# Performance work log

Measured on AMD Instinct MI355X. Metric: run time of the kernel, lower is better.

## Reference

```python
import jax, jax.numpy as jnp
import numpy as np

D_MODEL = 1024
N_HEADS = 16
D_KEY = 64
EPS = 1e-5


def setup_inputs() -> dict:
    key = jax.random.key(0)
    ks = jax.random.split(key, 12)
    d, h, dk = D_MODEL, N_HEADS, D_KEY
    s = lambda fan_in: 1.0 / np.sqrt(fan_in)
    inp = {
        "X": jax.random.normal(ks[0], (2, 2048, d), dtype=jnp.float32),
        "Wqkv": jax.random.uniform(ks[1], (d, 3 * h * dk), jnp.float32, -s(d), s(d)),
        "bqkv": jax.random.uniform(ks[2], (3 * h * dk,), jnp.float32, -s(d), s(d)),
        "Wo": jax.random.uniform(ks[3], (h * dk, d), jnp.float32, -s(h * dk), s(h * dk)),
        "bo": jax.random.uniform(ks[4], (d,), jnp.float32, -s(h * dk), s(h * dk)),
        "W1": jax.random.uniform(ks[5], (d, 4 * d), jnp.float32, -s(d), s(d)),
        "b1": jax.random.uniform(ks[6], (4 * d,), jnp.float32, -s(d), s(d)),
        "W2": jax.random.uniform(ks[7], (4 * d, d), jnp.float32, -s(4 * d), s(4 * d)),
        "b2": jax.random.uniform(ks[8], (d,), jnp.float32, -s(4 * d), s(4 * d)),
        "ln1_g": jnp.ones((d,), jnp.float32),
        "ln1_b": jnp.zeros((d,), jnp.float32),
        "ln2_g": jnp.ones((d,), jnp.float32),
        "ln2_b": jnp.zeros((d,), jnp.float32),
    }
    return inp


def _layernorm(x, g, b):
    mu = jnp.mean(x, axis=-1, keepdims=True)
    var = jnp.var(x, axis=-1, keepdims=True)
    return (x - mu) * jax.lax.rsqrt(var + EPS) * g + b


def _block(X, Wqkv, bqkv, Wo, bo, W1, b1, W2, b2, ln1_g, ln1_b, ln2_g, ln2_b):
    B, T, _ = X.shape
    h, dk = N_HEADS, D_KEY
    # --- causal multi-head self-attention on LN(X) ---
    Xn = _layernorm(X, ln1_g, ln1_b)
    qkv = (Xn @ Wqkv + bqkv).reshape(B, T, 3, h, dk)
    q, k, v = (jnp.moveaxis(qkv, 2, 0)[i].transpose(0, 2, 1, 3) for i in range(3))  # each [B,h,T,dk]
    scores = jnp.einsum("bhqd,bhkd->bhqk", q, k) / np.sqrt(dk).astype(np.float32)
    causal = jnp.tril(jnp.ones((T, T), dtype=bool))
    scores = jnp.where(causal, scores, -jnp.inf)
    attn = jax.nn.softmax(scores, axis=-1)
    ctx = jnp.einsum("bhqk,bhkd->bhqd", attn, v)  # [B,h,T,dk]
    ctx = ctx.transpose(0, 2, 1, 3).reshape(B, T, h * dk)
    atten = ctx @ Wo + bo
    X = X + atten  # dropout is identity in eval mode
    # --- FFN on LN(X) ---
    Xn2 = _layernorm(X, ln2_g, ln2_b)
    ffn = jax.nn.relu(Xn2 @ W1 + b1) @ W2 + b2
    return X + ffn


def reference(X, Wqkv, bqkv, Wo, bo, W1, b1, W2, b2, ln1_g, ln1_b, ln2_g, ln2_b):
    return _block(X, Wqkv, bqkv, Wo, bo, W1, b1, W2, b2, ln1_g, ln1_b, ln2_g, ln2_b)
```

## Files before the change

### kernel.cpp

```cpp
#include <hip/hip_runtime.h>
#include <hip/hip_bf16.h>

typedef __hip_bfloat16 bf16;
typedef __attribute__((ext_vector_type(8))) short short8;
typedef __attribute__((ext_vector_type(4))) float f32x4;

constexpr int D     = 1024;
constexpr int T     = 2048;
constexpr int BATCH = 2;
constexpr int ROWS  = BATCH * T;
constexpr int NH    = 16;
constexpr int DKEY  = 64;
constexpr int QKVN  = 3 * D;
constexpr int FFNN  = 4 * D;

static __device__ __forceinline__ float b2f(bf16 x) { return __bfloat162float(x); }
static __device__ __forceinline__ bf16  f2b(float x) { return __float2bfloat16(x); }
static __device__ __forceinline__ float fast_exp2(float x) { return __builtin_amdgcn_exp2f(x); }
static __device__ __forceinline__ unsigned short f2bu(float x) {
    return __bfloat16_as_ushort(__float2bfloat16(x));
}
static __device__ __forceinline__ float bits2f(unsigned short u) {
    unsigned int w = (unsigned int)u << 16;
    return __builtin_bit_cast(float, w);
}

static __device__ __forceinline__ void gload_lds16(const bf16* g, unsigned short* l) {
    __builtin_amdgcn_global_load_lds(
        (const __attribute__((address_space(1))) void*)g,
        (__attribute__((address_space(3))) void*)l,
        16, 0, 0);
}

__global__ __launch_bounds__(256) void transpose_cast(const float* __restrict__ in,
                                                      bf16* __restrict__ out,
                                                      int R, int C)
{
    __shared__ float tile[32][33];
    int c0 = blockIdx.x * 32, r0 = blockIdx.y * 32;
    int tx = threadIdx.x & 31, ty = threadIdx.x >> 5;
#pragma unroll
    for (int i = 0; i < 32; i += 8)
        tile[ty + i][tx] = in[(size_t)(r0 + ty + i) * C + c0 + tx];
    __syncthreads();
#pragma unroll
    for (int i = 0; i < 32; i += 8)
        out[(size_t)(c0 + ty + i) * R + r0 + tx] = f2b(tile[tx][ty + i]);
}

template <typename TIN>
__global__ __launch_bounds__(256) void ln_kernel(const TIN* __restrict__ X,
                                                 const float* __restrict__ g,
                                                 const float* __restrict__ b,
                                                 bf16* __restrict__ out)
{
    int row = blockIdx.x;
    int tid = threadIdx.x;
    int c0  = tid * 4;
    const TIN* xr = X + (size_t)row * D;
    float v[4];
    if constexpr (__is_same(TIN, float)) {
        float4 ld = *(const float4*)(xr + c0);
        v[0] = ld.x; v[1] = ld.y; v[2] = ld.z; v[3] = ld.w;
    } else {
        uint2 raw = *(const uint2*)(xr + c0);
        v[0] = bits2f((unsigned short)(raw.x & 0xffff));
        v[1] = bits2f((unsigned short)(raw.x >> 16));
        v[2] = bits2f((unsigned short)(raw.y & 0xffff));
        v[3] = bits2f((unsigned short)(raw.y >> 16));
    }

    float s1 = v[0] + v[1] + v[2] + v[3];
    float s2 = v[0]*v[0] + v[1]*v[1] + v[2]*v[2] + v[3]*v[3];
#pragma unroll
    for (int off = 32; off; off >>= 1) {
        s1 += __shfl_xor(s1, off);
        s2 += __shfl_xor(s2, off);
    }
    __shared__ float red[8];
    int lane = tid & 63, w = tid >> 6;
    if (lane == 0) { red[w] = s1; red[4 + w] = s2; }
    __syncthreads();
    s1 = red[0] + red[1] + red[2] + red[3];
    s2 = red[4] + red[5] + red[6] + red[7];

    float mu   = s1 * (1.0f / D);
    float var  = s2 * (1.0f / D) - mu * mu;
    float rstd = rsqrtf(var + 1e-5f);

    float4 gv = *(const float4*)(g + c0);
    float4 bv = *(const float4*)(b + c0);
    ushort4 pk;
    pk.x = f2bu((v[0] - mu) * rstd * gv.x + bv.x);
    pk.y = f2bu((v[1] - mu) * rstd * gv.y + bv.y);
    pk.z = f2bu((v[2] - mu) * rstd * gv.z + bv.z);
    pk.w = f2bu((v[3] - mu) * rstd * gv.w + bv.w);
    *(ushort4*)(out + (size_t)row * D + c0) = pk;
}

template <int BM, int RELU, int RES, int OUTF32, int SPLITZ>
__global__ __launch_bounds__(256) void mfma_gemm(
    const bf16* __restrict__ A, const bf16* __restrict__ Bt,
    const float* __restrict__ bias, const void* __restrict__ resid,
    void* __restrict__ out, float* __restrict__ part,
    int M, int N, int K, int Kstride)
{
    constexpr int MT = BM / 32;
    __shared__ __align__(16) unsigned short As[2][BM * 32];
    __shared__ __align__(16) unsigned short Bs[2][128 * 32];

    int gx = gridDim.x, gy = gridDim.y;
    int lid = (blockIdx.z * gy + blockIdx.y) * gx + blockIdx.x;
    int nwg = gx * gy * gridDim.z;
    int chunk = nwg >> 3;
    int xcd = lid & 7, c = lid >> 3;
    int f;
    if ((gx & 7) == 0 && chunk % (gx * 4) == 0) {
        int band  = c / (gx * 4);
        int r     = c % (gx * 4);
        int wi    = r >> 5;
        int inner = r & 31;
        f = xcd * chunk + band * (gx * 4) + (inner >> 3) * gx + wi * 8 + (inner & 7);
    } else {
        f = xcd * chunk + c;
    }
    int bx = f % gx;
    int by = (f / gx) % gy;
    int bz = f / (gx * gy);

    int tid  = threadIdx.x;
    int m0   = by * BM, n0 = bx * 128;
    int lane = tid & 63, wave = tid >> 6;
    int wm = (wave >> 1) * (MT * 16), wn = (wave & 1) * 64;
    int c15 = lane & 15, quad = lane >> 4;

    int koff = 0;
    if constexpr (SPLITZ) koff = bz * K;

    f32x4 acc[MT][4] = {};

    int srow = lane >> 2;
    int scol = (lane & 3) * 8;
    const bf16* abase = A  + (size_t)m0 * Kstride + koff;
    const bf16* bbase = Bt + (size_t)n0 * Kstride + koff;

    auto stage = [&](int buf, int kt) {
        int ko = kt * 32;
#pragma unroll
        for (int j = 0; j < 2; ++j) {
            int r = wave * 32 + j * 16;
            gload_lds16(bbase + (size_t)(r + srow) * Kstride + ko + scol,
                        &Bs[buf][r * 32]);
        }
        if constexpr (BM == 128) {
#pragma unroll
            for (int j = 0; j < 2; ++j) {
                int r = wave * 32 + j * 16;
                gload_lds16(abase + (size_t)(r + srow) * Kstride + ko + scol,
                            &As[buf][r * 32]);
            }
        } else {
            int r = wave * 16;
            gload_lds16(abase + (size_t)(r + srow) * Kstride + ko + scol,
                        &As[buf][r * 32]);
        }
    };

    int nk = K >> 5;
    stage(0, 0);
    __syncthreads();

    for (int kt = 0; kt < nk; ++kt) {
        int buf = kt & 1;
        if (kt + 1 < nk) stage(buf ^ 1, kt + 1);

        short8 af[MT], bfr[4];
#pragma unroll
        for (int t = 0; t < MT; ++t)
            af[t]  = *(const short8*)&As[buf][(wm + t * 16 + c15) * 32 + quad * 8];
#pragma unroll
        for (int t = 0; t < 4; ++t)
            bfr[t] = *(const short8*)&Bs[buf][(wn + t * 16 + c15) * 32 + quad * 8];
#pragma unroll
        for (int mt = 0; mt < MT; ++mt)
#pragma unroll
            for (int nt = 0; nt < 4; ++nt)
                acc[mt][nt] = __builtin_amdgcn_mfma_f32_16x16x32_bf16(
                    af[mt], bfr[nt], acc[mt][nt], 0, 0, 0);

        __syncthreads();
    }

#pragma unroll
    for (int mt = 0; mt < MT; ++mt) {
#pragma unroll
        for (int nt = 0; nt < 4; ++nt) {
            f32x4 v4 = acc[mt][nt];
            int gc = n0 + wn + nt * 16 + c15;
            float bb = (!SPLITZ || bz == 0) ? bias[gc] : 0.0f;
#pragma unroll
            for (int r = 0; r < 4; ++r) {
                int gr = m0 + wm + mt * 16 + quad * 4 + r;
                float v = v4[r] + bb;
                if constexpr (RELU) v = fmaxf(v, 0.0f);
                size_t idx = (size_t)gr * N + gc;
                if constexpr (SPLITZ) {
                    if (bz == 0) {
                        v += b2f(((const bf16*)resid)[idx]);
                        ((float*)out)[idx] = v;
                    } else {
                        part[idx] = v;
                    }
                } else {
                    if constexpr (RES == 1) v += b2f(((const bf16*)resid)[idx]);
                    if constexpr (RES == 2) v += ((const float*)resid)[idx];
                    if constexpr (OUTF32) ((float*)out)[idx] = v;
                    else                  ((bf16*)out)[idx] = f2b(v);
                }
            }
        }
    }
}

__global__ __launch_bounds__(256) void add_partial(float* __restrict__ out,
                                                   const float* __restrict__ part)
{
    int i = blockIdx.x * 256 + threadIdx.x;
    f32x4 a = ((const f32x4*)out)[i];
    f32x4 p = ((const f32x4*)part)[i];
    a += p;
    ((f32x4*)out)[i] = a;
}

__global__ __launch_bounds__(256) void flash_attn(const bf16* __restrict__ qkv,
                                                  bf16* __restrict__ ctx)
{
    constexpr int KROW = 72;
    constexpr float CSC = 0.18033688011112042f;
    constexpr float MSH = 12.0f;

    __shared__ __align__(16) unsigned short Qs[64 * KROW];
    __shared__ __align__(16) unsigned short Ks[64 * KROW];
    __shared__ __align__(16) unsigned short Vt[64 * KROW];
    unsigned short* Pt = Qs;

    int bx = blockIdx.x;
    int bh = bx & 31;
    int qi = 31 - (bx >> 5);
    int h  = bh & 15, b = bh >> 4;
    int q0 = qi * 64;

    int tid = threadIdx.x, lane = tid & 63, w = tid >> 6;
    int c15 = lane & 15, quad = lane >> 4;

    const bf16* base = qkv + (size_t)b * T * QKVN;

    {
        int row = tid >> 2, qtr = tid & 3;
        const bf16* src = base + (size_t)(q0 + row) * QKVN + h * 64 + qtr * 16;
        unsigned short* dst = &Qs[row * KROW + qtr * 16];
        uint4 v0 = *(const uint4*)(src);
        uint4 v1 = *(const uint4*)(src + 8);
        *(uint4*)(dst)     = v0;
        *(uint4*)(dst + 8) = v1;
    }
    __syncthreads();

    short8 qf[2];
#pragma unroll
    for (int s = 0; s < 2; ++s)
        qf[s] = *(const short8*)&Qs[(w * 16 + c15) * KROW + s * 32 + quad * 8];

    short8 ones;
#pragma unroll
    for (int i = 0; i < 8; ++i) ones[i] = (short)0x3F80;

    f32x4 Ot[4] = {};
    f32x4 lacc  = {};

    int nkt   = q0 / 64 + 1;
    int wqmin = q0 + w * 16;

    int key = tid >> 2, seg = tid & 3;
    int keyp = (tid & 31) * 2, dk0 = (tid >> 5) * 8;

    uint4 kv0, kv1, vv0, vv1;
    {
        const bf16* ksrc = base + (size_t)key * QKVN + D + h * 64 + seg * 16;
        kv0 = *(const uint4*)ksrc;
        kv1 = *(const uint4*)(ksrc + 8);
        const bf16* vsrc = base + (size_t)keyp * QKVN + 2 * D + h * 64 + dk0;
        vv0 = *(const uint4*)vsrc;
        vv1 = *(const uint4*)(vsrc + QKVN);
    }

    for (int kt = 0; kt < nkt; ++kt) {
        int k0 = kt * 64;

        __syncthreads();
        {
            unsigned short* kd = &Ks[key * KROW + seg * 16];
            *(uint4*)kd       = kv0;
            *(uint4*)(kd + 8) = kv1;
            const unsigned short* lo = (const unsigned short*)&vv0;
            const unsigned short* hi = (const unsigned short*)&vv1;
#pragma unroll
            for (int j = 0; j < 8; ++j) {
                unsigned int pk = (unsigned int)lo[j] | ((unsigned int)hi[j] << 16);
                *(unsigned int*)&Vt[(dk0 + j) * KROW + keyp] = pk;
            }
        }
        __syncthreads();

        if (kt + 1 < nkt) {
            int k1 = k0 + 64;
            const bf16* ksrc = base + (size_t)(k1 + key) * QKVN + D + h * 64 + seg * 16;
            kv0 = *(const uint4*)ksrc;
            kv1 = *(const uint4*)(ksrc + 8);
            const bf16* vsrc = base + (size_t)(k1 + keyp) * QKVN + 2 * D + h * 64 + dk0;
            vv0 = *(const uint4*)vsrc;
            vv1 = *(const uint4*)(vsrc + QKVN);
        }

        f32x4 St[4] = {};
        __builtin_amdgcn_s_setprio(1);
#pragma unroll
        for (int s = 0; s < 2; ++s)
#pragma unroll
            for (int ktm = 0; ktm < 4; ++ktm) {
                short8 kf = *(const short8*)&Ks[(ktm * 16 + c15) * KROW + s * 32 + quad * 8];
                St[ktm] = __builtin_amdgcn_mfma_f32_16x16x32_bf16(kf, qf[s], St[ktm], 0, 0, 0);
            }
        __builtin_amdgcn_s_setprio(0);

        if (kt == nkt - 1) {
            int q_g = wqmin + c15;
#pragma unroll
            for (int ktm = 0; ktm < 4; ++ktm) {
                ushort4 pk;
#pragma unroll
                for (int r = 0; r < 4; ++r) {
                    float p = fast_exp2(fmaf(St[ktm][r], CSC, -MSH));
                    if (k0 + ktm * 16 + quad * 4 + r > q_g) p = 0.0f;
                    ((unsigned short*)&pk)[r] = f2bu(p);
                }
                *(ushort4*)&Pt[(w * 16 + c15) * KROW + ktm * 16 + quad * 4] = pk;
            }
        } else {
#pragma unroll
            for (int ktm = 0; ktm < 4; ++ktm) {
                ushort4 pk;
#pragma unroll
                for (int r = 0; r < 4; ++r)
                    ((unsigned short*)&pk)[r] = f2bu(fast_exp2(fmaf(St[ktm][r], CSC, -MSH)));
                *(ushort4*)&Pt[(w * 16 + c15) * KROW + ktm * 16 + quad * 4] = pk;
            }
        }

        __builtin_amdgcn_s_setprio(1);
#pragma unroll
        for (int s = 0; s < 2; ++s) {
            short8 pf = *(const short8*)&Pt[(w * 16 + c15) * KROW + s * 32 + quad * 8];
            lacc = __builtin_amdgcn_mfma_f32_16x16x32_bf16(ones, pf, lacc, 0, 0, 0);
#pragma unroll
            for (int dt = 0; dt < 4; ++dt) {
                short8 vf = *(const short8*)&Vt[(dt * 16 + c15) * KROW + s * 32 + quad * 8];
                Ot[dt] = __builtin_amdgcn_mfma_f32_16x16x32_bf16(vf, pf, Ot[dt], 0, 0, 0);
            }
        }
        __builtin_amdgcn_s_setprio(0);
    }

    {
        float inv = 1.0f / lacc[0];
        int grow = b * T + q0 + w * 16 + c15;
        bf16* dst = ctx + (size_t)grow * D + h * 64 + quad * 4;
#pragma unroll
        for (int dt = 0; dt < 4; ++dt) {
            ushort4 pk;
#pragma unroll
            for (int r = 0; r < 4; ++r)
                ((unsigned short*)&pk)[r] = f2bu(Ot[dt][r] * inv);
            *(ushort4*)(dst + dt * 16) = pk;
        }
    }
}

extern "C" void kernel_launch(void* const* d_in, const int* in_sizes, int n_in,
                              void* d_out, int out_size, void* d_ws, size_t ws_size,
                              hipStream_t stream)
{
    const float* X    = (const float*)d_in[0];
    const float* Wqkv = (const float*)d_in[1];
    const float* bqkv = (const float*)d_in[2];
    const float* Wo   = (const float*)d_in[3];
    const float* bo   = (const float*)d_in[4];
    const float* W1   = (const float*)d_in[5];
    const float* b1   = (const float*)d_in[6];
    const float* W2   = (const float*)d_in[7];
    const float* b2   = (const float*)d_in[8];
    const float* ln1g = (const float*)d_in[9];
    const float* ln1b = (const float*)d_in[10];
    const float* ln2g = (const float*)d_in[11];
    const float* ln2b = (const float*)d_in[12];
    float* out = (float*)d_out;

    char* ws = (char*)d_ws;
    bf16* Wqkv_t = (bf16*)(ws + 0);
    bf16* Wo_t   = (bf16*)(ws + 6291456);
    bf16* W1_t   = (bf16*)(ws + 8388608);
    bf16* W2_t   = (bf16*)(ws + 16777216);
    bf16* Xn     = (bf16*)(ws + 25165824);
    bf16* X1     = Xn;
    bf16* qkv    = (bf16*)(ws + 33554432);
    bf16* Xn2    = (bf16*)(ws + 33554432);
    bf16* ctx    = (bf16*)(ws + 58720256);
    bf16* mid    = (bf16*)(ws + 41943040);
    float* W2part = (float*)(ws + 0);

    transpose_cast<<<dim3(QKVN / 32, D / 32), 256, 0, stream>>>(Wqkv, Wqkv_t, D, QKVN);
    transpose_cast<<<dim3(D / 32, D / 32), 256, 0, stream>>>(Wo, Wo_t, D, D);
    transpose_cast<<<dim3(FFNN / 32, D / 32), 256, 0, stream>>>(W1, W1_t, D, FFNN);
    transpose_cast<<<dim3(D / 32, FFNN / 32), 256, 0, stream>>>(W2, W2_t, FFNN, D);

    ln_kernel<float><<<ROWS, 256, 0, stream>>>(X, ln1g, ln1b, Xn);
    mfma_gemm<128, 0, 0, 0, 0><<<dim3(QKVN / 128, ROWS / 128), 256, 0, stream>>>(
        Xn, Wqkv_t, bqkv, nullptr, qkv, nullptr, ROWS, QKVN, D, D);
    flash_attn<<<1024, 256, 0, stream>>>(qkv, ctx);
    mfma_gemm<64, 0, 2, 0, 0><<<dim3(D / 128, ROWS / 64), 256, 0, stream>>>(
        ctx, Wo_t, bo, X, X1, nullptr, ROWS, D, D, D);
    ln_kernel<bf16><<<ROWS, 256, 0, stream>>>(X1, ln2g, ln2b, Xn2);
    mfma_gemm<128, 1, 0, 0, 0><<<dim3(FFNN / 128, ROWS / 128), 256, 0, stream>>>(
        Xn2, W1_t, b1, nullptr, mid, nullptr, ROWS, FFNN, D, D);
    mfma_gemm<64, 0, 1, 1, 1><<<dim3(D / 128, ROWS / 64, 2), 256, 0, stream>>>(
        mid, W2_t, b2, X1, out, W2part, ROWS, D, FFNN / 2, FFNN);
    add_partial<<<ROWS * D / 4 / 256, 256, 0, stream>>>(out, W2part);
}
```

Before: 349.9 us.

## Add 256x256 tiled MFMA GEMM with LDS swizzle for the FFN up-projection

Replaces the generic 128-tile GEMM for the FFN first layer (with ReLU) with a dedicated kernel. It uses 256x256 output tiles, 512 threads, double-buffered XOR-swizzled LDS filled by direct global-to-LDS loads, and staging of the next K tile interleaved with the MFMA phases under raised wave priority. The larger tile cuts global and LDS traffic per FLOP, and the overlap is meant to hide load latency. The generic GEMM's block swizzle is also reduced to a plain XCD-chunk mapping, which drops the band-grouping locality scheme. The 128 KB of dynamic LDS limits occupancy to one block per CU and may need LDS-size support on the target.

```diff
diff --git a/kernel.cpp b/kernel.cpp
--- a/kernel.cpp
+++ b/kernel.cpp
@@ -113,20 +113,10 @@
     int lid = (blockIdx.z * gy + blockIdx.y) * gx + blockIdx.x;
     int nwg = gx * gy * gridDim.z;
     int chunk = nwg >> 3;
-    int xcd = lid & 7, c = lid >> 3;
-    int f;
-    if ((gx & 7) == 0 && chunk % (gx * 4) == 0) {
-        int band  = c / (gx * 4);
-        int r     = c % (gx * 4);
-        int wi    = r >> 5;
-        int inner = r & 31;
-        f = xcd * chunk + band * (gx * 4) + (inner >> 3) * gx + wi * 8 + (inner & 7);
-    } else {
-        f = xcd * chunk + c;
-    }
-    int bx = f % gx;
-    int by = (f / gx) % gy;
-    int bz = f / (gx * gy);
+    int swz = (lid & 7) * chunk + (lid >> 3);
+    int bx = swz % gx;
+    int by = (swz / gx) % gy;
+    int bz = swz / (gx * gy);
 
     int tid  = threadIdx.x;
     int m0   = by * BM, n0 = bx * 128;
@@ -222,6 +212,117 @@
     }
 }
 
+__global__ __launch_bounds__(512, 2) void gemm256_relu(
+    const bf16* __restrict__ A, const bf16* __restrict__ Bt,
+    const float* __restrict__ bias, bf16* __restrict__ out,
+    int M, int N, int K)
+{
+    extern __shared__ unsigned short smem[];
+    unsigned short* Abase = smem;
+    unsigned short* Bbase = smem + 32768;
+
+    int gx = gridDim.x;
+    int lid = blockIdx.y * gx + blockIdx.x;
+    int nwg = gx * gridDim.y;
+    int chunk = nwg >> 3;
+    int f = (lid & 7) * chunk + (lid >> 3);
+    int bx = f % gx, by = f / gx;
+
+    int tid  = threadIdx.x;
+    int m0   = by * 256, n0 = bx * 256;
+    int lane = tid & 63, wave = tid >> 6;
+    int wm = wave >> 2;
+    int wn = (wave & 3) * 64;
+    int c15 = lane & 15, quad = lane >> 4;
+
+    int rloc  = lane >> 3;
+    int sslot = (lane & 7) ^ (rloc & 7);
+
+    auto stageA = [&](int bufo, int k4, int ko) {
+        int r0 = k4 * 64 + wave * 8;
+        const bf16* g = A + (size_t)(m0 + r0 + rloc) * K + ko + sslot * 8;
+        gload_lds16(g, Abase + bufo + r0 * 64);
+    };
+    auto stageB = [&](int bufo, int k4, int ko) {
+        int r0 = k4 * 64 + wave * 8;
+        const bf16* g = Bt + (size_t)(n0 + r0 + rloc) * K + ko + sslot * 8;
+        gload_lds16(g, Bbase + bufo + r0 * 64);
+    };
+    auto ldf = [&](const unsigned short* base, int row, int kq) {
+        int slot = kq ^ (row & 7);
+        return *(const short8*)&base[row * 64 + slot * 8];
+    };
+
+    f32x4 acc[8][4] = {};
+
+    int nt = K >> 6;
+#pragma unroll
+    for (int k4 = 0; k4 < 4; ++k4) stageA(0, k4, 0);
+#pragma unroll
+    for (int k4 = 0; k4 < 4; ++k4) stageB(0, k4, 0);
+
+    for (int t = 0; t < nt; ++t) {
+        int co = (t & 1) * 16384, no = co ^ 16384;
+        bool more = (t + 1 < nt);
+        int ko1 = (t + 1) * 64;
+        const unsigned short* Ac = Abase + co;
+        const unsigned short* Bc = Bbase + co;
+
+        if (more) {
+            stageA(no, 0, ko1);
+            stageA(no, 1, ko1);
+            asm volatile("s_waitcnt vmcnt(2)" ::: "memory");
+        } else {
+            asm volatile("s_waitcnt vmcnt(0)" ::: "memory");
+        }
+        __builtin_amdgcn_s_barrier();
+
+#pragma unroll
+        for (int p = 0; p < 4; ++p) {
+            const int mh = p >> 1, kq0 = (p & 1) * 4 + quad;
+            short8 af[4], bf[4];
+#pragma unroll
+            for (int i = 0; i < 4; ++i)
+                af[i] = ldf(Ac, wm * 128 + mh * 64 + i * 16 + c15, kq0);
+#pragma unroll
+            for (int j = 0; j < 4; ++j)
+                bf[j] = ldf(Bc, wn + j * 16 + c15, kq0);
+            if (more) {
+                if (p == 0) { stageA(no, 2, ko1); stageA(no, 3, ko1); }
+                if (p == 1) { stageB(no, 0, ko1); stageB(no, 1, ko1); }
+                if (p == 2) { stageB(no, 2, ko1); stageB(no, 3, ko1); }
+            }
+            __builtin_amdgcn_s_barrier();
+            asm volatile("s_waitcnt lgkmcnt(0)" ::: "memory");
+            __builtin_amdgcn_sched_barrier(0);
+            __builtin_amdgcn_s_setprio(1);
+#pragma unroll
+            for (int i = 0; i < 4; ++i)
+#pragma unroll
+                for (int j = 0; j < 4; ++j)
+                    acc[mh * 4 + i][j] = __builtin_amdgcn_mfma_f32_16x16x32_bf16(
+                        af[i], bf[j], acc[mh * 4 + i][j], 0, 0, 0);
+            __builtin_amdgcn_s_setprio(0);
+            __builtin_amdgcn_s_barrier();
+        }
+    }
+
+#pragma unroll
+    for (int fr = 0; fr < 8; ++fr) {
+#pragma unroll
+        for (int j = 0; j < 4; ++j) {
+            int gc = n0 + wn + j * 16 + c15;
+            float bb = bias[gc];
+#pragma unroll
+            for (int r = 0; r < 4; ++r) {
+                int gr = m0 + wm * 128 + fr * 16 + quad * 4 + r;
+                float v = fmaxf(acc[fr][j][r] + bb, 0.0f);
+                out[(size_t)gr * N + gc] = f2b(v);
+            }
+        }
+    }
+}
+
 __global__ __launch_bounds__(256) void add_partial(float* __restrict__ out,
                                                    const float* __restrict__ part)
 {
@@ -430,8 +531,8 @@
     mfma_gemm<64, 0, 2, 0, 0><<<dim3(D / 128, ROWS / 64), 256, 0, stream>>>(
         ctx, Wo_t, bo, X, X1, nullptr, ROWS, D, D, D);
     ln_kernel<bf16><<<ROWS, 256, 0, stream>>>(X1, ln2g, ln2b, Xn2);
-    mfma_gemm<128, 1, 0, 0, 0><<<dim3(FFNN / 128, ROWS / 128), 256, 0, stream>>>(
-        Xn2, W1_t, b1, nullptr, mid, nullptr, ROWS, FFNN, D, D);
+    gemm256_relu<<<dim3(FFNN / 256, ROWS / 256), 512, 131072, stream>>>(
+        Xn2, W1_t, b1, mid, ROWS, FFNN, D);
     mfma_gemm<64, 0, 1, 1, 1><<<dim3(D / 128, ROWS / 64, 2), 256, 0, stream>>>(
         mid, W2_t, b2, X1, out, W2part, ROWS, D, FFNN / 2, FFNN);
     add_partial<<<ROWS * D / 4 / 256, 256, 0, stream>>>(out, W2part);
```

Result: faster. 335.6 us (-4.1%).
